# Kernel optimization log

Measured on AMD Instinct MI355X. Metric: run time of the kernel, lower is better.

The kernel has to match this reference:

```python
import jax, jax.numpy as jnp
import numpy as np

T, H, E, I, K = 4096, 1024, 16, 768, 8  # tokens, hidden, experts, intermediate, top_k


def setup_inputs() -> dict:
    key = jax.random.key(0)
    k0, k1, k2, k3, k4 = jax.random.split(key, 5)
    scale = 0.02
    return {
        "hidden_states": jax.random.normal(k0, (T, H), dtype=jnp.float32),
        "gate_w": jax.random.normal(k1, (H, E), dtype=jnp.float32) * scale,
        "w1": jax.random.normal(k2, (E, H, I), dtype=jnp.float32) * scale,  # gate proj
        "w3": jax.random.normal(k3, (E, H, I), dtype=jnp.float32) * scale,  # up proj
        "w2": jax.random.normal(k4, (E, I, H), dtype=jnp.float32) * scale,  # down proj
    }


def reference(hidden_states, gate_w, w1, w3, w2):
    x = hidden_states  # [T, H]
    # Router: replicated linear (no bias) -> softmax -> top-k -> renormalize
    router_logits = x @ gate_w  # [T, E]
    probs = jax.nn.softmax(router_logits.astype(jnp.float32), axis=-1)
    topk_w, topk_idx = jax.lax.top_k(probs, K)  # [T, K]
    topk_w = topk_w / jnp.sum(topk_w, axis=-1, keepdims=True)  # norm_topk_prob=True
    # Dense routing-weight matrix [T, E]: zero for non-selected experts
    dense_w = jnp.zeros((T, E), dtype=x.dtype)
    dense_w = dense_w.at[jnp.arange(T)[:, None], topk_idx].set(topk_w.astype(x.dtype))
    # SwiGLU experts, computed densely over experts and masked by routing weights
    h = jnp.einsum("th,ehi->tei", x, w1)  # [T, E, I]
    u = jnp.einsum("th,ehi->tei", x, w3)  # [T, E, I]
    act = jax.nn.silu(h) * u  # [T, E, I]
    out = jnp.einsum("tei,eih,te->th", act, w2, dense_w)  # weighted combine -> [T, H]
    return out
```

## Files before the change

### kernel.cpp

```cpp
#include <hip/hip_runtime.h>
#include <hip/hip_bf16.h>

#define T_ 4096
#define H_ 1024
#define E_ 16
#define I_ 768
#define KTOP 8
#define MAXSLOT 4096
#define ACT_ROWS 34816

typedef __attribute__((ext_vector_type(8))) short bf16x8;
typedef __attribute__((ext_vector_type(4))) float f32x4;

__device__ __forceinline__ unsigned short f2bf(float f) {
  unsigned u = __builtin_bit_cast(unsigned, f);
  u += 0x7fff + ((u >> 16) & 1);
  return (unsigned short)(u >> 16);
}

typedef __attribute__((address_space(3))) void lds_void;
typedef __attribute__((address_space(1))) void g_void;

__device__ __forceinline__ void gload_lds16(const void* g, void* l) {
  __builtin_amdgcn_global_load_lds((g_void*)g, (lds_void*)l, 16, 0, 0);
}

__global__ void router_kernel(const float* __restrict__ x,
                              const float* __restrict__ gate_w,
                              int* __restrict__ cnt,
                              int* __restrict__ tok_list,
                              float* __restrict__ rw_list) {
  int t = blockIdx.x;
  int lane = threadIdx.x;
  int e = lane & 15;
  int chunk = lane >> 4;
  const float* xr = x + (size_t)t * H_;
  int h0 = chunk * 256;
  float partial = 0.f;
  for (int i = 0; i < 256; i += 4) {
    float4 xv = *reinterpret_cast<const float4*>(xr + h0 + i);
    partial += xv.x * gate_w[(size_t)(h0 + i    ) * E_ + e];
    partial += xv.y * gate_w[(size_t)(h0 + i + 1) * E_ + e];
    partial += xv.z * gate_w[(size_t)(h0 + i + 2) * E_ + e];
    partial += xv.w * gate_w[(size_t)(h0 + i + 3) * E_ + e];
  }
  partial += __shfl_xor(partial, 16);
  partial += __shfl_xor(partial, 32);
  float logit = partial;
  float m = logit;
  for (int d = 1; d < 16; d <<= 1) m = fmaxf(m, __shfl_xor(m, d));
  float p = __expf(logit - m);
  int base = lane & ~15;
  int rank = 0;
  for (int j = 0; j < 16; ++j) {
    float pj = __shfl(p, base + j);
    rank += (pj > p) || (pj == p && j < e);
  }
  bool sel = rank < KTOP;
  float contrib = sel ? p : 0.f;
  float s = contrib;
  for (int d = 1; d < 16; d <<= 1) s += __shfl_xor(s, d);
  float w = sel ? p / s : 0.f;
  if (lane < 16 && sel) {
    int slot = atomicAdd(&cnt[e], 1);
    tok_list[e * MAXSLOT + slot] = t;
    rw_list[e * MAXSLOT + slot] = w;
  }
}

__global__ void offsets_kernel(const int* __restrict__ cnt,
                               int* __restrict__ off,
                               int* __restrict__ ntiles) {
  int acc = 0;
  for (int e = 0; e < E_; ++e) {
    off[e] = acc;
    int nt = (cnt[e] + 127) >> 7;
    ntiles[e] = nt;
    acc += nt << 7;
  }
}

__global__ void cast_x_kernel(const float* __restrict__ x,
                              unsigned short* __restrict__ xb) {
  int idx = blockIdx.x * blockDim.x + threadIdx.x;
  float4 v = reinterpret_cast<const float4*>(x)[idx];
  ushort4 o;
  o.x = f2bf(v.x); o.y = f2bf(v.y); o.z = f2bf(v.z); o.w = f2bf(v.w);
  *reinterpret_cast<ushort4*>(xb + (size_t)idx * 4) = o;
}

__global__ void transpose_w13_kernel(const float* __restrict__ w1,
                                     const float* __restrict__ w3,
                                     unsigned short* __restrict__ w1t,
                                     unsigned short* __restrict__ w3t) {
  __shared__ float tile[64][65];
  int i0 = blockIdx.x * 64;
  int h0 = blockIdx.y * 64;
  int e = blockIdx.z & 15;
  const float* src = (blockIdx.z < 16 ? w1 : w3) + (size_t)e * H_ * I_;
  unsigned short* dst = (blockIdx.z < 16 ? w1t : w3t) + (size_t)e * I_ * H_;
  int tx = threadIdx.x & 63, ty = threadIdx.x >> 6;
  for (int r = 0; r < 64; r += 4)
    tile[ty + r][tx] = src[(size_t)(h0 + ty + r) * I_ + i0 + tx];
  __syncthreads();
  for (int r = 0; r < 64; r += 4) {
    int i = ty + r;
    dst[(size_t)(i0 + i) * H_ + h0 + tx] = f2bf(tile[tx][i]);
  }
}

__global__ void transpose_w2_kernel(const float* __restrict__ w2,
                                    unsigned short* __restrict__ w2te) {
  __shared__ float tile[64][65];
  int h0 = blockIdx.x * 64;
  int i0 = blockIdx.y * 64;
  int e = blockIdx.z;
  const float* src = w2 + (size_t)e * I_ * H_;
  int tx = threadIdx.x & 63, ty = threadIdx.x >> 6;
  for (int r = 0; r < 64; r += 4)
    tile[ty + r][tx] = src[(size_t)(i0 + ty + r) * H_ + h0 + tx];
  __syncthreads();
  for (int r = 0; r < 64; r += 4) {
    int h = ty + r;
    w2te[((size_t)e * H_ + h0 + h) * I_ + i0 + tx] = f2bf(tile[tx][h]);
  }
}

__global__ __launch_bounds__(256) void moe_up_kernel(
    const unsigned short* __restrict__ xb,
    const unsigned short* __restrict__ w1t,
    const unsigned short* __restrict__ w3t,
    const int* __restrict__ tok_list,
    const float* __restrict__ rw_list,
    const int* __restrict__ off,
    const int* __restrict__ ntiles,
    unsigned short* __restrict__ act_g) {
  const int e = blockIdx.z;
  const int tile = blockIdx.x;
  if (tile >= ntiles[e]) return;

  __shared__ __align__(16) unsigned short Asm[128 * 32];
  __shared__ __align__(16) unsigned short B1sm[64 * 32];
  __shared__ __align__(16) unsigned short B3sm[64 * 32];
  __shared__ int tok_sm[128];
  __shared__ float rw_sm[128];

  const int col0 = blockIdx.y * 64;
  const int tid = threadIdx.x;
  const int lane = tid & 63;
  const int w = tid >> 6;
  const int wm = w >> 1, wn = w & 1;
  const int slot0 = off[e] + tile * 128;

  if (tid < 128) {
    int li = e * MAXSLOT + tile * 128 + tid;
    tok_sm[tid] = tok_list[li];
    rw_sm[tid] = rw_list[li];
  }
  __syncthreads();

  const int r_in_chunk = lane >> 2;
  const int kpart = (lane & 3) * 8;

  const unsigned short* asrc[4];
  if (w < 2) {
#pragma unroll
    for (int i = 0; i < 4; ++i) {
      int row = (w * 4 + i) * 16 + r_in_chunk;
      asrc[i] = xb + (size_t)tok_sm[row] * H_ + kpart;
    }
  }
  const unsigned short* B1base = w1t + ((size_t)e * I_ + col0) * H_;
  const unsigned short* B3base = w3t + ((size_t)e * I_ + col0) * H_;

  f32x4 acc1[4][2] = {};
  f32x4 acc2[4][2] = {};

  const int lrow = lane & 15;
  const int lk = (lane >> 4) * 8;

  for (int k0 = 0; k0 < H_; k0 += 32) {
    if (w < 2) {
#pragma unroll
      for (int i = 0; i < 4; ++i)
        gload_lds16(asrc[i] + k0, &Asm[(w * 4 + i) * 512]);
    } else if (w == 2) {
#pragma unroll
      for (int i = 0; i < 4; ++i) {
        int row = i * 16 + r_in_chunk;
        gload_lds16(B1base + (size_t)row * H_ + k0 + kpart, &B1sm[i * 512]);
      }
    } else {
#pragma unroll
      for (int i = 0; i < 4; ++i) {
        int row = i * 16 + r_in_chunk;
        gload_lds16(B3base + (size_t)row * H_ + k0 + kpart, &B3sm[i * 512]);
      }
    }
    __syncthreads();
    bf16x8 af[4], b1f[2], b3f[2];
    for (int m = 0; m < 4; ++m)
      af[m] = *reinterpret_cast<const bf16x8*>(&Asm[(wm * 64 + m * 16 + lrow) * 32 + lk]);
    for (int n = 0; n < 2; ++n) {
      b1f[n] = *reinterpret_cast<const bf16x8*>(&B1sm[(wn * 32 + n * 16 + lrow) * 32 + lk]);
      b3f[n] = *reinterpret_cast<const bf16x8*>(&B3sm[(wn * 32 + n * 16 + lrow) * 32 + lk]);
    }
    for (int m = 0; m < 4; ++m)
      for (int n = 0; n < 2; ++n) {
        acc1[m][n] = __builtin_amdgcn_mfma_f32_16x16x32_bf16(af[m], b1f[n], acc1[m][n], 0, 0, 0);
        acc2[m][n] = __builtin_amdgcn_mfma_f32_16x16x32_bf16(af[m], b3f[n], acc2[m][n], 0, 0, 0);
      }
    __syncthreads();
  }

  const int crow = (lane >> 4) * 4;
  const int ccol = lane & 15;
  for (int m = 0; m < 4; ++m)
    for (int n = 0; n < 2; ++n)
      for (int r = 0; r < 4; ++r) {
        int rl = wm * 64 + m * 16 + crow + r;
        int cl = wn * 32 + n * 16 + ccol;
        float hv = acc1[m][n][r];
        float uv = acc2[m][n][r];
        float a = (hv / (1.f + __expf(-hv))) * uv * rw_sm[rl];
        act_g[(size_t)(slot0 + rl) * I_ + col0 + cl] = f2bf(a);
      }
}

__global__ __launch_bounds__(256) void moe_down_kernel(
    const unsigned short* __restrict__ act_g,
    const unsigned short* __restrict__ w2te,
    const int* __restrict__ tok_list,
    const int* __restrict__ off,
    const int* __restrict__ ntiles,
    float* __restrict__ out) {
  const int e = blockIdx.z;
  const int tile = blockIdx.x;
  if (tile >= ntiles[e]) return;

  __shared__ __align__(16) unsigned short Asm[128 * 32];
  __shared__ __align__(16) unsigned short Bsm[128 * 32];
  __shared__ int tok_sm[128];

  const int col0 = blockIdx.y * 128;
  const int tid = threadIdx.x;
  const int lane = tid & 63;
  const int w = tid >> 6;
  const int wm = w >> 1, wn = w & 1;

  if (tid < 128) tok_sm[tid] = tok_list[e * MAXSLOT + tile * 128 + tid];

  const int r_in_chunk = lane >> 2;
  const int kpart = (lane & 3) * 8;

  const unsigned short* Abase = act_g + (size_t)(off[e] + tile * 128) * I_;
  const unsigned short* Bbase = w2te + ((size_t)e * H_ + col0) * I_;

  f32x4 acc[4][4] = {};

  const int lrow = lane & 15;
  const int lk = (lane >> 4) * 8;

  for (int k0 = 0; k0 < I_; k0 += 32) {
    for (int i = 0; i < 2; ++i) {
      int c = w * 2 + i;
      int row = c * 16 + r_in_chunk;
      gload_lds16(Abase + (size_t)row * I_ + k0 + kpart, &Asm[c * 512]);
      gload_lds16(Bbase + (size_t)row * I_ + k0 + kpart, &Bsm[c * 512]);
    }
    __syncthreads();
    bf16x8 af[4], bf[4];
    for (int m = 0; m < 4; ++m)
      af[m] = *reinterpret_cast<const bf16x8*>(&Asm[(wm * 64 + m * 16 + lrow) * 32 + lk]);
    for (int n = 0; n < 4; ++n)
      bf[n] = *reinterpret_cast<const bf16x8*>(&Bsm[(wn * 64 + n * 16 + lrow) * 32 + lk]);
    for (int m = 0; m < 4; ++m)
      for (int n = 0; n < 4; ++n)
        acc[m][n] = __builtin_amdgcn_mfma_f32_16x16x32_bf16(af[m], bf[n], acc[m][n], 0, 0, 0);
    __syncthreads();
  }

  const int crow = (lane >> 4) * 4;
  const int ccol = lane & 15;
  for (int m = 0; m < 4; ++m)
    for (int n = 0; n < 4; ++n)
      for (int r = 0; r < 4; ++r) {
        int rl = wm * 64 + m * 16 + crow + r;
        int cl = wn * 64 + n * 16 + ccol;
        atomicAdd(&out[(size_t)tok_sm[rl] * H_ + col0 + cl], acc[m][n][r]);
      }
}

extern "C" void kernel_launch(void* const* d_in, const int* in_sizes, int n_in,
                              void* d_out, int out_size, void* d_ws, size_t ws_size,
                              hipStream_t stream) {
  const float* x      = (const float*)d_in[0];
  const float* gate_w = (const float*)d_in[1];
  const float* w1     = (const float*)d_in[2];
  const float* w3     = (const float*)d_in[3];
  const float* w2     = (const float*)d_in[4];
  float* out = (float*)d_out;

  int* ctrl     = (int*)d_ws;
  int* cnt      = ctrl;
  int* off      = ctrl + 16;
  int* ntiles   = ctrl + 32;
  int* tok_list = ctrl + 64;
  float* rw_list = (float*)(tok_list + E_ * MAXSLOT);
  unsigned short* xb   = (unsigned short*)(rw_list + E_ * MAXSLOT);
  unsigned short* w1t  = xb  + (size_t)T_ * H_;
  unsigned short* w3t  = w1t + (size_t)E_ * I_ * H_;
  unsigned short* w2te = w3t + (size_t)E_ * I_ * H_;
  unsigned short* act_g = w2te + (size_t)E_ * H_ * I_;

  hipMemsetAsync(d_ws, 0, (64 + 2 * E_ * MAXSLOT) * sizeof(int), stream);
  hipMemsetAsync(d_out, 0, (size_t)T_ * H_ * sizeof(float), stream);

  router_kernel<<<T_, 64, 0, stream>>>(x, gate_w, cnt, tok_list, rw_list);
  offsets_kernel<<<1, 1, 0, stream>>>(cnt, off, ntiles);
  cast_x_kernel<<<(T_ * H_ / 4) / 256, 256, 0, stream>>>(x, xb);
  transpose_w13_kernel<<<dim3(I_ / 64, H_ / 64, 32), 256, 0, stream>>>(w1, w3, w1t, w3t);
  transpose_w2_kernel<<<dim3(H_ / 64, I_ / 64, E_), 256, 0, stream>>>(w2, w2te);
  moe_up_kernel<<<dim3(32, I_ / 64, E_), 256, 0, stream>>>(
      xb, w1t, w3t, tok_list, rw_list, off, ntiles, act_g);
  moe_down_kernel<<<dim3(32, H_ / 128, E_), 256, 0, stream>>>(
      act_g, w2te, tok_list, off, ntiles, out);
}
```

Measured before the change: 774.2 us.

## Replace atomic scatter in down projection with bf16 staging and gather combine

The down-projection kernel now writes per-slot results as bf16 into a staging buffer instead of issuing fp32 atomicAdds into the output. A new combine kernel gathers each token's eight expert rows through a token-to-slot map recorded by the router and sums them. This removes the output memset and atomic contention, at the cost of an extra kernel and staging traffic. Rounding partial outputs to bf16 before summation adds some precision loss, and the staging buffer reuses the w1t/w3t region after the up kernel finishes.

```diff
diff --git a/kernel.cpp b/kernel.cpp
--- a/kernel.cpp
+++ b/kernel.cpp
@@ -17,6 +17,10 @@
   u += 0x7fff + ((u >> 16) & 1);
   return (unsigned short)(u >> 16);
 }
+__device__ __forceinline__ float bf2f(unsigned short u) {
+  unsigned v = ((unsigned)u) << 16;
+  return __builtin_bit_cast(float, v);
+}
 
 typedef __attribute__((address_space(3))) void lds_void;
 typedef __attribute__((address_space(1))) void g_void;
@@ -29,7 +33,8 @@
                               const float* __restrict__ gate_w,
                               int* __restrict__ cnt,
                               int* __restrict__ tok_list,
-                              float* __restrict__ rw_list) {
+                              float* __restrict__ rw_list,
+                              int* __restrict__ tok2es) {
   int t = blockIdx.x;
   int lane = threadIdx.x;
   int e = lane & 15;
@@ -65,6 +70,7 @@
     int slot = atomicAdd(&cnt[e], 1);
     tok_list[e * MAXSLOT + slot] = t;
     rw_list[e * MAXSLOT + slot] = w;
+    tok2es[t * KTOP + rank] = (e << 20) | slot;
   }
 }
 
@@ -230,30 +236,27 @@
 __global__ __launch_bounds__(256) void moe_down_kernel(
     const unsigned short* __restrict__ act_g,
     const unsigned short* __restrict__ w2te,
-    const int* __restrict__ tok_list,
     const int* __restrict__ off,
     const int* __restrict__ ntiles,
-    float* __restrict__ out) {
+    unsigned short* __restrict__ dout_g) {
   const int e = blockIdx.z;
   const int tile = blockIdx.x;
   if (tile >= ntiles[e]) return;
 
   __shared__ __align__(16) unsigned short Asm[128 * 32];
   __shared__ __align__(16) unsigned short Bsm[128 * 32];
-  __shared__ int tok_sm[128];
 
   const int col0 = blockIdx.y * 128;
   const int tid = threadIdx.x;
   const int lane = tid & 63;
   const int w = tid >> 6;
   const int wm = w >> 1, wn = w & 1;
-
-  if (tid < 128) tok_sm[tid] = tok_list[e * MAXSLOT + tile * 128 + tid];
+  const int slot0 = off[e] + tile * 128;
 
   const int r_in_chunk = lane >> 2;
   const int kpart = (lane & 3) * 8;
 
-  const unsigned short* Abase = act_g + (size_t)(off[e] + tile * 128) * I_;
+  const unsigned short* Abase = act_g + (size_t)slot0 * I_;
   const unsigned short* Bbase = w2te + ((size_t)e * H_ + col0) * I_;
 
   f32x4 acc[4][4] = {};
@@ -287,8 +290,34 @@
       for (int r = 0; r < 4; ++r) {
         int rl = wm * 64 + m * 16 + crow + r;
         int cl = wn * 64 + n * 16 + ccol;
-        atomicAdd(&out[(size_t)tok_sm[rl] * H_ + col0 + cl], acc[m][n][r]);
-      }
+        dout_g[(size_t)(slot0 + rl) * H_ + col0 + cl] = f2bf(acc[m][n][r]);
+      }
+}
+
+__global__ __launch_bounds__(256) void combine_kernel(
+    const unsigned short* __restrict__ dout_g,
+    const int* __restrict__ tok2es,
+    const int* __restrict__ off,
+    float* __restrict__ out) {
+  __shared__ int gs[KTOP];
+  int t = blockIdx.x;
+  if (threadIdx.x < KTOP) {
+    int es = tok2es[t * KTOP + threadIdx.x];
+    int e = es >> 20, s = es & 0xFFFFF;
+    gs[threadIdx.x] = off[e] + s;
+  }
+  __syncthreads();
+  int h = threadIdx.x * 4;
+  float4 sum = {0.f, 0.f, 0.f, 0.f};
+#pragma unroll
+  for (int k = 0; k < KTOP; ++k) {
+    ushort4 v = *reinterpret_cast<const ushort4*>(&dout_g[(size_t)gs[k] * H_ + h]);
+    sum.x += bf2f(v.x);
+    sum.y += bf2f(v.y);
+    sum.z += bf2f(v.z);
+    sum.w += bf2f(v.w);
+  }
+  *reinterpret_cast<float4*>(&out[(size_t)t * H_ + h]) = sum;
 }
 
 extern "C" void kernel_launch(void* const* d_in, const int* in_sizes, int n_in,
@@ -301,22 +330,24 @@
   const float* w2     = (const float*)d_in[4];
   float* out = (float*)d_out;
 
-  int* ctrl     = (int*)d_ws;
+  char* ws = (char*)d_ws;
+  int* ctrl     = (int*)ws;
   int* cnt      = ctrl;
   int* off      = ctrl + 16;
   int* ntiles   = ctrl + 32;
   int* tok_list = ctrl + 64;
   float* rw_list = (float*)(tok_list + E_ * MAXSLOT);
-  unsigned short* xb   = (unsigned short*)(rw_list + E_ * MAXSLOT);
-  unsigned short* w1t  = xb  + (size_t)T_ * H_;
-  unsigned short* w3t  = w1t + (size_t)E_ * I_ * H_;
-  unsigned short* w2te = w3t + (size_t)E_ * I_ * H_;
+  int* tok2es   = (int*)(rw_list + E_ * MAXSLOT);
+  unsigned short* xb    = (unsigned short*)(ws + (1 << 20));
+  unsigned short* w2te  = xb + (size_t)T_ * H_;
   unsigned short* act_g = w2te + (size_t)E_ * H_ * I_;
-
-  hipMemsetAsync(d_ws, 0, (64 + 2 * E_ * MAXSLOT) * sizeof(int), stream);
-  hipMemsetAsync(d_out, 0, (size_t)T_ * H_ * sizeof(float), stream);
-
-  router_kernel<<<T_, 64, 0, stream>>>(x, gate_w, cnt, tok_list, rw_list);
+  unsigned short* w1t   = act_g + (size_t)ACT_ROWS * I_;
+  unsigned short* w3t   = w1t + (size_t)E_ * I_ * H_;
+  unsigned short* dout_g = w1t;
+
+  hipMemsetAsync(d_ws, 0, (64 + 2 * E_ * MAXSLOT + T_ * KTOP) * sizeof(int), stream);
+
+  router_kernel<<<T_, 64, 0, stream>>>(x, gate_w, cnt, tok_list, rw_list, tok2es);
   offsets_kernel<<<1, 1, 0, stream>>>(cnt, off, ntiles);
   cast_x_kernel<<<(T_ * H_ / 4) / 256, 256, 0, stream>>>(x, xb);
   transpose_w13_kernel<<<dim3(I_ / 64, H_ / 64, 32), 256, 0, stream>>>(w1, w3, w1t, w3t);
@@ -324,5 +355,6 @@
   moe_up_kernel<<<dim3(32, I_ / 64, E_), 256, 0, stream>>>(
       xb, w1t, w3t, tok_list, rw_list, off, ntiles, act_g);
   moe_down_kernel<<<dim3(32, H_ / 128, E_), 256, 0, stream>>>(
-      act_g, w2te, tok_list, off, ntiles, out);
-}
+      act_g, w2te, off, ntiles, dout_g);
+  combine_kernel<<<T_, 256, 0, stream>>>(dout_g, tok2es, off, out);
+}
```

After: 620.5 us. 19.9% less time.
